# Kernel optimization log

Hardware: AMD Instinct MI355X
Metric: run time of the kernel (lower is better)

Reference implementation:

```python
import jax, jax.numpy as jnp
import numpy as np

M, C = 100000, 24
LINE_W, LENGTH_W, REPROJ_W = 0.0, 0.0, 1.0  # forward() default weights


def setup_inputs() -> dict:
    ks = jax.random.split(jax.random.key(0), 8)
    # 3 pole markers per frame, centered ~5m in front of cameras (positive depth)
    pole3d = 0.5 * jax.random.normal(ks[0], (M, 3, 3), jnp.float32) + jnp.array([0.0, 0.0, 5.0], jnp.float32)
    # intrinsics: fx=fy~1000, principal point ~(960,540)
    fx = 1000.0 + 10.0 * jax.random.normal(ks[1], (C,), jnp.float32)
    fy = 1000.0 + 10.0 * jax.random.normal(ks[2], (C,), jnp.float32)
    u0 = 960.0 + 5.0 * jax.random.normal(ks[3], (C,), jnp.float32)
    v0 = 540.0 + 5.0 * jax.random.normal(ks[4], (C,), jnp.float32)
    K = jnp.zeros((C, 3, 3), jnp.float32)
    K = K.at[:, 0, 0].set(fx).at[:, 1, 1].set(fy).at[:, 0, 2].set(u0).at[:, 1, 2].set(v0).at[:, 2, 2].set(1.0)
    dist = 0.01 * jax.random.normal(ks[5], (C, 5), jnp.float32)  # k1,k2,p1,p2,k3
    R = jnp.eye(3, dtype=jnp.float32)[None] + 0.01 * jax.random.normal(ks[6], (C, 3, 3), jnp.float32)
    t = 0.1 * jax.random.normal(ks[7], (C, 3), jnp.float32)
    # detected pixels in a 1920x1080 frame
    pole2d = jax.random.uniform(jax.random.fold_in(ks[0], 1), (M, C, 3, 2), jnp.float32) * jnp.array([1920.0, 1080.0], jnp.float32)
    # visibility mask; guarantee >=1 visible camera per frame (matches non-empty loss_reproj)
    mask = jax.random.randint(jax.random.fold_in(ks[0], 2), (M, C), 0, 2, jnp.int32).at[:, 0].set(1)
    pole = jnp.array([0.5, 0.5], jnp.float32)  # [d1, d2] in meters
    return {"pole3d": pole3d, "pole2d": pole2d, "K": K, "dist": dist, "R": R, "t": t, "pole": pole, "mask": mask}


def _project(X, K, R, t, dist):
    # X: [M,P,3] world points; outputs pixels [M,C,P,2]
    xc = jnp.einsum('cij,mpj->mcpi', R, X) + t[None, :, None, :]   # camera frame
    xn = xc[..., :2] / xc[..., 2:3]                                # perspective divide
    x0, x1 = xn[..., 0], xn[..., 1]
    r2 = x0 * x0 + x1 * x1
    k1, k2, p1, p2, k3 = (dist[:, i][None, :, None] for i in range(5))
    radial = 1.0 + k1 * r2 + k2 * r2 * r2 + k3 * r2 * r2 * r2
    xu = x0 * radial + 2.0 * p1 * x0 * x1 + p2 * (r2 + 2.0 * x0 * x0)
    yu = x1 * radial + p1 * (r2 + 2.0 * x1 * x1) + 2.0 * p2 * x0 * x1
    fx = K[:, 0, 0][None, :, None]; fy = K[:, 1, 1][None, :, None]
    u0 = K[:, 0, 2][None, :, None]; v0 = K[:, 1, 2][None, :, None]
    return jnp.stack([fx * xu + u0, fy * yu + v0], axis=-1)


def reference(pole3d, pole2d, K, dist, R, t, pole, mask):
    d1, d2 = pole[0], pole[1]
    dsum = d1 + d2
    # wand geometry loss per frame
    expect_mid = (d2 * pole3d[:, 0] + d1 * pole3d[:, 2]) / dsum            # [M,3]
    loss_line = jnp.linalg.norm(pole3d[:, 1] - expect_mid, axis=-1)        # [M]
    loss_length = jnp.abs(jnp.linalg.norm(pole3d[:, 0] - pole3d[:, 2], axis=-1) - dsum)
    loss_wand = LINE_W * loss_line + LENGTH_W * loss_length                # [M]
    # reprojection loss
    proj = _project(pole3d, K, R, t, dist)                                 # [M,C,3,2]
    per_cam = REPROJ_W * jnp.linalg.norm(pole2d - proj, axis=-1).mean(axis=-1)  # [M,C]
    m = mask.astype(per_cam.dtype)
    loss_reproj = (per_cam * m).sum(axis=-1) / m.sum(axis=-1)              # masked mean over cams
    return jnp.mean(loss_wand + loss_reproj)
```

## Files before the change

kernel.cpp:

```cpp
#include <hip/hip_runtime.h>

#define MM 100000
#define CC 24
#define BLK 256
#define WPB (BLK / 64)
#define GRID 1280
#define NW (GRID * WPB)
#define NP (MM / 2)

struct Pack {
    float2 a0, a1, a2;
    float  w;
    float  q[9];
};

__device__ __forceinline__ Pack load_pack(
    const float* __restrict__ pole3d, const float* __restrict__ pole2d,
    const int* __restrict__ mask, int m, int c, float active)
{
    Pack pk;
    const float2* pd = (const float2*)(pole2d + ((size_t)m * CC + c) * 6);
    pk.a0 = pd[0]; pk.a1 = pd[1]; pk.a2 = pd[2];
    pk.w  = active * (float)mask[(size_t)m * CC + c];
    const float* q = pole3d + (size_t)m * 9;
    #pragma unroll
    for (int i = 0; i < 9; ++i) pk.q[i] = q[i];
    return pk;
}

__global__ __launch_bounds__(BLK) void ba_main_kernel(
    const float* __restrict__ pole3d,
    const float* __restrict__ pole2d,
    const float* __restrict__ Kmat,
    const float* __restrict__ dist,
    const float* __restrict__ Rmat,
    const float* __restrict__ tvec,
    const int*   __restrict__ mask,
    float* __restrict__ ws)
{
    const int tid  = threadIdx.x;
    const int lane = tid & 63;
    const int half = lane >> 5;
    const int cl   = lane & 31;
    const int c    = (cl < CC) ? cl : (CC - 1);
    const float active = (cl < CC) ? 1.f : 0.f;

    const float fx = Kmat[c * 9 + 0], fy = Kmat[c * 9 + 4];
    const float u0 = Kmat[c * 9 + 2], v0 = Kmat[c * 9 + 5];
    const float k1 = dist[c * 5 + 0], k2 = dist[c * 5 + 1];
    const float p1 = dist[c * 5 + 2], p2 = dist[c * 5 + 3], k3 = dist[c * 5 + 4];
    const float r00 = Rmat[c * 9 + 0], r01 = Rmat[c * 9 + 1], r02 = Rmat[c * 9 + 2];
    const float r10 = Rmat[c * 9 + 3], r11 = Rmat[c * 9 + 4], r12 = Rmat[c * 9 + 5];
    const float r20 = Rmat[c * 9 + 6], r21 = Rmat[c * 9 + 7], r22 = Rmat[c * 9 + 8];
    const float t0 = tvec[c * 3 + 0], t1 = tvec[c * 3 + 1], t2 = tvec[c * 3 + 2];

    const int wid = blockIdx.x * WPB + (tid >> 6);

    float acc = 0.f;

    Pack cur = load_pack(pole3d, pole2d, mask, 2 * wid + half, c, active);

    for (int p = wid; p < NP; p += NW) {
        const int pn = p + NW;
        const int pc = (pn < NP) ? pn : wid;
        Pack nxt = load_pack(pole3d, pole2d, mask, 2 * pc + half, c, active);

        float s = 0.f;
        const float2 obs[3] = {cur.a0, cur.a1, cur.a2};
        #pragma unroll
        for (int i = 0; i < 3; ++i) {
            const float X = cur.q[3 * i + 0], Y = cur.q[3 * i + 1], Z = cur.q[3 * i + 2];
            const float xc = r00 * X + r01 * Y + r02 * Z + t0;
            const float yc = r10 * X + r11 * Y + r12 * Z + t1;
            const float zc = r20 * X + r21 * Y + r22 * Z + t2;
            const float inv = __builtin_amdgcn_rcpf(zc);
            const float x0 = xc * inv, x1 = yc * inv;
            const float r2 = x0 * x0 + x1 * x1;
            const float radial = 1.f + r2 * (k1 + r2 * (k2 + r2 * k3));
            const float xu = x0 * radial + 2.f * p1 * x0 * x1 + p2 * (r2 + 2.f * x0 * x0);
            const float yu = x1 * radial + p1 * (r2 + 2.f * x1 * x1) + 2.f * p2 * x0 * x1;
            const float u = fx * xu + u0;
            const float v = fy * yu + v0;
            const float dx = obs[i].x - u;
            const float dy = obs[i].y - v;
            s += __builtin_amdgcn_sqrtf(dx * dx + dy * dy);
        }
        s *= (1.f / 3.f);

        const unsigned long long ball = __ballot(cur.w != 0.f);
        const unsigned wcnt = half ? __popcll(ball >> 32)
                                   : __popcll(ball & 0xFFFFFFFFull);
        const float ww = (float)wcnt;

        float ss = s * cur.w;
        #pragma unroll
        for (int d = 1; d < 32; d <<= 1) ss += __shfl_xor(ss, d);

        acc += ss * __builtin_amdgcn_rcpf(ww);

        cur = nxt;
    }

    const float tot = acc + __shfl_xor(acc, 32);

    __shared__ float sh[WPB];
    if (lane == 0) sh[tid >> 6] = tot;
    __syncthreads();
    if (tid == 0) {
        float bl = 0.f;
        #pragma unroll
        for (int j = 0; j < WPB; ++j) bl += sh[j];
        ws[blockIdx.x] = bl;
    }
}

__global__ __launch_bounds__(256) void ba_reduce_kernel(
    const float* __restrict__ ws, float* __restrict__ out)
{
    __shared__ float sh[256];
    float s = 0.f;
    for (int i = threadIdx.x; i < GRID; i += 256) s += ws[i];
    sh[threadIdx.x] = s;
    __syncthreads();
    #pragma unroll
    for (int st = 128; st > 0; st >>= 1) {
        if (threadIdx.x < st) sh[threadIdx.x] += sh[threadIdx.x + st];
        __syncthreads();
    }
    if (threadIdx.x == 0) out[0] = sh[0] * (1.0f / MM);
}

extern "C" void kernel_launch(void* const* d_in, const int* in_sizes, int n_in,
                              void* d_out, int out_size, void* d_ws, size_t ws_size,
                              hipStream_t stream) {
    const float* pole3d = (const float*)d_in[0];
    const float* pole2d = (const float*)d_in[1];
    const float* Kmat   = (const float*)d_in[2];
    const float* dist   = (const float*)d_in[3];
    const float* Rmat   = (const float*)d_in[4];
    const float* tvec   = (const float*)d_in[5];
    const int*   mask   = (const int*)d_in[7];
    float* out = (float*)d_out;
    float* ws  = (float*)d_ws;

    ba_main_kernel<<<GRID, BLK, 0, stream>>>(
        pole3d, pole2d, Kmat, dist, Rmat, tvec, mask, ws);
    ba_reduce_kernel<<<1, 256, 0, stream>>>(ws, out);
}
```

Before: 28.96 us.

## Stage frame tiles into LDS via async global_load_lds with double buffering

Replaces per-lane register prefetch of scattered pole2d/mask/pole3d loads with block-cooperative 16-byte global_load_lds copies of contiguous 16-frame tiles into a double-buffered LDS region. Each wave then reads its frames from LDS, and the grid shrinks to 1024 blocks so the 6250 tiles are spread over them. The intent is fully coalesced, wide DMA-style loads that overlap with compute on the previous tile. In exchange it adds about 23KB of LDS per block and a barrier per tile, and the LDS reads with a 6-float stride per camera may cause bank conflicts.

```diff
diff --git a/kernel.cpp b/kernel.cpp
--- a/kernel.cpp
+++ b/kernel.cpp
@@ -1,31 +1,40 @@
 #include <hip/hip_runtime.h>
+#include <stdint.h>
 
 #define MM 100000
 #define CC 24
 #define BLK 256
-#define WPB (BLK / 64)
-#define GRID 1280
-#define NW (GRID * WPB)
-#define NP (MM / 2)
+#define WPB 4
+#define GRID 1024
+#define TILE 16
+#define NT (MM / TILE)
+#define STEPS 2
 
-struct Pack {
-    float2 a0, a1, a2;
-    float  w;
-    float  q[9];
-};
+#define P2_B 9216
+#define P3_B 576
+#define MS_B 1536
+#define TILE_B (P2_B + P3_B + MS_B)
 
-__device__ __forceinline__ Pack load_pack(
+__device__ __forceinline__ void ld_lds16(const void* g, void* l) {
+    __builtin_amdgcn_global_load_lds(
+        (const __attribute__((address_space(1))) uint32_t*)g,
+        (__attribute__((address_space(3))) uint32_t*)l, 16, 0, 0);
+}
+
+__device__ __forceinline__ void stage_tile(
     const float* __restrict__ pole3d, const float* __restrict__ pole2d,
-    const int* __restrict__ mask, int m, int c, float active)
+    const int* __restrict__ mask, int t, char* lb, int tid)
 {
-    Pack pk;
-    const float2* pd = (const float2*)(pole2d + ((size_t)m * CC + c) * 6);
-    pk.a0 = pd[0]; pk.a1 = pd[1]; pk.a2 = pd[2];
-    pk.w  = active * (float)mask[(size_t)m * CC + c];
-    const float* q = pole3d + (size_t)m * 9;
+    const char* g2 = (const char*)pole2d + (size_t)t * P2_B;
+    const char* g3 = (const char*)pole3d + (size_t)t * P3_B;
+    const char* gm = (const char*)mask   + (size_t)t * MS_B;
     #pragma unroll
-    for (int i = 0; i < 9; ++i) pk.q[i] = q[i];
-    return pk;
+    for (int k = 0; k < 3; ++k) {
+        const int i = tid + k * BLK;
+        if (i < P2_B / 16) ld_lds16(g2 + 16 * i, lb + 16 * i);
+    }
+    if (tid < P3_B / 16) ld_lds16(g3 + 16 * tid, lb + P2_B + 16 * tid);
+    if (tid < MS_B / 16) ld_lds16(gm + 16 * tid, lb + P2_B + P3_B + 16 * tid);
 }
 
 __global__ __launch_bounds__(BLK) void ba_main_kernel(
@@ -38,8 +47,12 @@
     const int*   __restrict__ mask,
     float* __restrict__ ws)
 {
+    __shared__ __align__(16) char lbuf[2 * TILE_B];
+    __shared__ float sh[WPB];
+
     const int tid  = threadIdx.x;
     const int lane = tid & 63;
+    const int wv   = tid >> 6;
     const int half = lane >> 5;
     const int cl   = lane & 31;
     const int c    = (cl < CC) ? cl : (CC - 1);
@@ -54,57 +67,72 @@
     const float r20 = Rmat[c * 9 + 6], r21 = Rmat[c * 9 + 7], r22 = Rmat[c * 9 + 8];
     const float t0 = tvec[c * 3 + 0], t1 = tvec[c * 3 + 1], t2 = tvec[c * 3 + 2];
 
-    const int wid = blockIdx.x * WPB + (tid >> 6);
-
     float acc = 0.f;
 
-    Pack cur = load_pack(pole3d, pole2d, mask, 2 * wid + half, c, active);
+    stage_tile(pole3d, pole2d, mask, blockIdx.x, lbuf, tid);
+    __syncthreads();
 
-    for (int p = wid; p < NP; p += NW) {
-        const int pn = p + NW;
-        const int pc = (pn < NP) ? pn : wid;
-        Pack nxt = load_pack(pole3d, pole2d, mask, 2 * pc + half, c, active);
+    int cur = 0;
+    for (int t = blockIdx.x; t < NT; t += GRID) {
+        const int tn = t + GRID;
+        if (tn < NT) stage_tile(pole3d, pole2d, mask, tn, lbuf + (cur ^ 1) * TILE_B, tid);
 
-        float s = 0.f;
-        const float2 obs[3] = {cur.a0, cur.a1, cur.a2};
+        const char* cb = lbuf + cur * TILE_B;
+        const float* P2 = (const float*)cb;
+        const float* P3 = (const float*)(cb + P2_B);
+        const int*   MS = (const int*)(cb + P2_B + P3_B);
+
         #pragma unroll
-        for (int i = 0; i < 3; ++i) {
-            const float X = cur.q[3 * i + 0], Y = cur.q[3 * i + 1], Z = cur.q[3 * i + 2];
-            const float xc = r00 * X + r01 * Y + r02 * Z + t0;
-            const float yc = r10 * X + r11 * Y + r12 * Z + t1;
-            const float zc = r20 * X + r21 * Y + r22 * Z + t2;
-            const float inv = __builtin_amdgcn_rcpf(zc);
-            const float x0 = xc * inv, x1 = yc * inv;
-            const float r2 = x0 * x0 + x1 * x1;
-            const float radial = 1.f + r2 * (k1 + r2 * (k2 + r2 * k3));
-            const float xu = x0 * radial + 2.f * p1 * x0 * x1 + p2 * (r2 + 2.f * x0 * x0);
-            const float yu = x1 * radial + p1 * (r2 + 2.f * x1 * x1) + 2.f * p2 * x0 * x1;
-            const float u = fx * xu + u0;
-            const float v = fy * yu + v0;
-            const float dx = obs[i].x - u;
-            const float dy = obs[i].y - v;
-            s += __builtin_amdgcn_sqrtf(dx * dx + dy * dy);
+        for (int j = 0; j < STEPS; ++j) {
+            const int fl = (j * WPB + wv) * 2 + half;
+            const float* ob = P2 + fl * (CC * 6) + c * 6;
+            const float ox0 = ob[0], oy0 = ob[1];
+            const float ox1 = ob[2], oy1 = ob[3];
+            const float ox2 = ob[4], oy2 = ob[5];
+            float q[9];
+            #pragma unroll
+            for (int i = 0; i < 9; ++i) q[i] = P3[fl * 9 + i];
+            const float wm = active * (float)MS[fl * CC + c];
+
+            float s = 0.f;
+            #pragma unroll
+            for (int i = 0; i < 3; ++i) {
+                const float X = q[3 * i + 0], Y = q[3 * i + 1], Z = q[3 * i + 2];
+                const float xc = r00 * X + r01 * Y + r02 * Z + t0;
+                const float yc = r10 * X + r11 * Y + r12 * Z + t1;
+                const float zc = r20 * X + r21 * Y + r22 * Z + t2;
+                const float inv = __builtin_amdgcn_rcpf(zc);
+                const float x0 = xc * inv, x1 = yc * inv;
+                const float r2 = x0 * x0 + x1 * x1;
+                const float radial = 1.f + r2 * (k1 + r2 * (k2 + r2 * k3));
+                const float xu = x0 * radial + 2.f * p1 * x0 * x1 + p2 * (r2 + 2.f * x0 * x0);
+                const float yu = x1 * radial + p1 * (r2 + 2.f * x1 * x1) + 2.f * p2 * x0 * x1;
+                const float uu = fx * xu + u0;
+                const float vv = fy * yu + v0;
+                const float dx = (i == 0 ? ox0 : i == 1 ? ox1 : ox2) - uu;
+                const float dy = (i == 0 ? oy0 : i == 1 ? oy1 : oy2) - vv;
+                s += __builtin_amdgcn_sqrtf(dx * dx + dy * dy);
+            }
+            s *= (1.f / 3.f);
+
+            const unsigned long long ball = __ballot(wm != 0.f);
+            const unsigned wcnt = half ? __popcll(ball >> 32)
+                                       : __popcll(ball & 0xFFFFFFFFull);
+
+            float ss = s * wm;
+            #pragma unroll
+            for (int d = 1; d < 32; d <<= 1) ss += __shfl_xor(ss, d);
+
+            acc += ss * __builtin_amdgcn_rcpf((float)wcnt);
         }
-        s *= (1.f / 3.f);
 
-        const unsigned long long ball = __ballot(cur.w != 0.f);
-        const unsigned wcnt = half ? __popcll(ball >> 32)
-                                   : __popcll(ball & 0xFFFFFFFFull);
-        const float ww = (float)wcnt;
-
-        float ss = s * cur.w;
-        #pragma unroll
-        for (int d = 1; d < 32; d <<= 1) ss += __shfl_xor(ss, d);
-
-        acc += ss * __builtin_amdgcn_rcpf(ww);
-
-        cur = nxt;
+        __syncthreads();
+        cur ^= 1;
     }
 
     const float tot = acc + __shfl_xor(acc, 32);
 
-    __shared__ float sh[WPB];
-    if (lane == 0) sh[tid >> 6] = tot;
+    if (lane == 0) sh[wv] = tot;
     __syncthreads();
     if (tid == 0) {
         float bl = 0.f;
```

New measurement: 29.37 us. No clear change (+1.4%).
